# Performance work log

Hardware: AMD Instinct MI355X
Metric: run time of the kernel (lower is better)

## Reference

```python
import jax, jax.numpy as jnp
import numpy as np

STRIDE = 1  # conv stride from __init__


def setup_inputs() -> dict:
    key = jax.random.key(0)
    k1, k2, k3 = jax.random.split(key, 3)
    prot1 = jax.random.normal(k1, (4, 1024, 8, 64), dtype=jnp.float32)
    prot2 = jax.random.normal(k2, (4, 1024, 8, 64), dtype=jnp.float32)
    # W: (no_filters, no_channels, no_dims, window_size)
    W = jax.random.normal(k3, (32, 8, 64, 7), dtype=jnp.float32)
    return {"prot1": prot1, "prot2": prot2, "W": W}


def _project(x, W, stride):
    """Fused equivalent of unfold + broadcast-mul + sum over (C, window).

    x: (N, H, C, D), W: (F, C, D, w) -> (N, F, H', D) with H' = (H - w)//stride + 1.
    This is a grouped 1D conv: D groups, each mixing C input channels into F outputs.
    """
    N, H, C, D = x.shape
    Fn, _, _, w = W.shape
    xg = jnp.transpose(x, (0, 3, 2, 1)).reshape(N, D * C, H)        # (N, D*C, H)
    Wg = jnp.transpose(W, (2, 0, 1, 3)).reshape(D * Fn, C, w)       # (D*F, C, w)
    out = jax.lax.conv_general_dilated(
        xg, Wg, window_strides=(stride,), padding='VALID',
        dimension_numbers=('NCH', 'OIH', 'NCH'), feature_group_count=D)
    Hp = out.shape[-1]
    return jnp.transpose(out.reshape(N, D, Fn, Hp), (0, 2, 3, 1))   # (N, F, H', D)


def reference(prot1, prot2, W):
    q1 = _project(prot1, W, STRIDE)   # (N, F, H1', D)
    q2 = _project(prot2, W, STRIDE)   # (N, F, H2', D)
    H1p, H2p = q1.shape[2], q2.shape[2]
    scale = jnp.sqrt(jnp.asarray(H1p * H2p, dtype=q1.dtype))
    att = jnp.einsum('nfhd,nfgd->nfhg', q1, q2) / scale             # (N, F, H1', H2')
    a = jax.nn.softmax(att, axis=3)
    p1 = jnp.einsum('nfhg,nfgd->nfhd', a, q2)                       # (N, F, H1', D)
    # NB: source does transpose(att, 2, 2) (a no-op) and multiplies the SAME
    # softmax matrix by the UPDATED p1folds; we reproduce that faithfully.
    p2 = jnp.einsum('nfhg,nfgd->nfhd', a, p1)                       # (N, F, H1', D)
    out1 = jnp.tanh(jnp.transpose(p1, (0, 2, 1, 3)))                # (N, H1', F, D)
    out2 = jnp.tanh(jnp.transpose(p2, (0, 2, 1, 3)))
    # Dropout is identity in eval mode (and dropout_p=0.0 here).
    return (out1, out2)
```

## Files before the change

kernel.cpp:

```cpp
#include <hip/hip_runtime.h>
#include <math.h>

typedef __bf16 bf16_t;
typedef bf16_t bf16x4 __attribute__((ext_vector_type(4)));
typedef bf16_t bf16x8 __attribute__((ext_vector_type(8)));
typedef float  f32x16 __attribute__((ext_vector_type(16)));

#define HH 1024
#define CC 8
#define DD 64
#define FF 32
#define WW 7
#define HP 1018
#define HPAD 1024
#define NF 128
#define QOUT (NF*HP*DD)
#define QWS ((size_t)NF*HPAD*DD)

#if __has_builtin(__builtin_amdgcn_exp2f)
#define EXP2(x) __builtin_amdgcn_exp2f(x)
#else
#define EXP2(x) __expf((x) * 0.6931471805599453f)
#endif

#define QSCALE (1.442695040888963f / 1018.f)

__device__ __forceinline__ int vaddr(int row, int col) {
    return row*64 + ((((col>>3) ^ (row&7) ^ ((row>>2)&7)))<<3) + (col&7);
}

__global__ __launch_bounds__(256) void wprep_kernel(
    const float* __restrict__ Wt, float* __restrict__ Wp)
{
    const int idx = blockIdx.x * 256 + threadIdx.x;
    if (idx < FF*CC*DD*WW) {
        const int j = idx % WW;
        int t = idx / WW;
        const int d = t % DD; t /= DD;
        const int c = t % CC;
        const int f = t / CC;
        Wp[((f*CC + c)*WW + j)*DD + d] = Wt[idx];
    }
}

__global__ __launch_bounds__(256, 3) void conv_kernel(
    const float* __restrict__ x1, const float* __restrict__ x2,
    const float* __restrict__ Wp, bf16_t* __restrict__ q1, bf16_t* __restrict__ q2)
{
    __shared__ float xs[22*512];
    const int zin = blockIdx.z & 1;
    const int fh = blockIdx.z >> 1;
    const float* x = zin ? x2 : x1;
    bf16_t* q = zin ? q2 : q1;
    const float qs = zin ? 1.f : QSCALE;
    const int n = blockIdx.y;
    const int hb = blockIdx.x * 16;
    const int tid = threadIdx.x;

    const float4* xg = (const float4*)(x + (size_t)n*HH*512);
    float4* xsv = (float4*)xs;
#pragma unroll
    for (int it = 0; it < 11; ++it) {
        const int i = it*256 + tid;
        const int row = hb + (i >> 7);
        float4 v = {0.f, 0.f, 0.f, 0.f};
        if (row < HH) v = xg[(size_t)row*128 + (i & 127)];
        xsv[i] = v;
    }

    const int d = tid & 63;
    const int fq = tid >> 6;

    float w[2][CC][WW];
#pragma unroll
    for (int fi = 0; fi < 2; ++fi) {
        const int f = fq*8 + fh*2 + fi;
#pragma unroll
        for (int c = 0; c < CC; ++c)
#pragma unroll
            for (int j = 0; j < WW; ++j)
                w[fi][c][j] = Wp[((f*CC + c)*WW + j)*DD + d];
    }

    __syncthreads();

    float acc[2][16];
#pragma unroll
    for (int fi = 0; fi < 2; ++fi)
#pragma unroll
        for (int i = 0; i < 16; ++i) acc[fi][i] = 0.f;

#pragma unroll
    for (int rr = 0; rr < 22; ++rr) {
        float xv[CC];
#pragma unroll
        for (int c = 0; c < CC; ++c)
            xv[c] = xs[rr*512 + c*64 + d];
#pragma unroll
        for (int fi = 0; fi < 2; ++fi)
#pragma unroll
            for (int j = 0; j < WW; ++j) {
                const int i = rr - j;
                if (i >= 0 && i < 16) {
#pragma unroll
                    for (int c = 0; c < CC; ++c)
                        acc[fi][i] = fmaf(xv[c], w[fi][c][j], acc[fi][i]);
                }
            }
    }

#pragma unroll
    for (int fi = 0; fi < 2; ++fi) {
        const int f = fq*8 + fh*2 + fi;
#pragma unroll
        for (int i = 0; i < 16; ++i) {
            const int h = hb + i;
            const float v = (h < HP) ? acc[fi][i]*qs : 0.f;
            q[((size_t)(n*FF + f)*HPAD + h)*DD + d] = (bf16_t)v;
        }
    }
}

__device__ __forceinline__ float fast_tanh(float x) {
    const float t = __expf(2.f * x);
    return (t - 1.f) / (t + 1.f);
}

#define MT_STEP(mtv) {                                                            \
    f32x16 C[2] = {};                                                             \
    __builtin_amdgcn_s_setprio(1);                                                \
    _Pragma("unroll")                                                             \
    for (int kt = 0; kt < 4; ++kt) {                                              \
        C[0] = __builtin_amdgcn_mfma_f32_32x32x16_bf16(aq[mtv][kt], bq1[0][kt], C[0], 0,0,0); \
        C[1] = __builtin_amdgcn_mfma_f32_32x32x16_bf16(aq[mtv][kt], bq1[1][kt], C[1], 0,0,0); \
    }                                                                             \
    __builtin_amdgcn_s_setprio(0);                                                \
    if (g0 + 64 < HPAD) {                                                         \
        _Pragma("unroll")                                                         \
        for (int kt = 0; kt < 4; ++kt)                                            \
            aq[mtv][kt] = *(const bf16x8*)&ap[(size_t)(g0 + 64 + 32*(mtv))*DD + 16*kt]; \
    }                                                                             \
    bf16x8 af[2][2];                                                              \
    _Pragma("unroll")                                                             \
    for (int nt = 0; nt < 2; ++nt) {                                              \
        float ls = 0.f;                                                           \
        _Pragma("unroll")                                                         \
        for (int s = 0; s < 16; ++s) {                                            \
            float e = EXP2(C[nt][s]);                                             \
            if (tail) {                                                           \
                const int gg = g0 + 32*(mtv) + (s&3) + 8*(s>>2) + 4*half;         \
                if (gg >= HP) e = 0.f;                                            \
            }                                                                     \
            ls += e;                                                              \
            af[nt][s>>3][s&7] = (bf16_t)e;                                        \
        }                                                                         \
        lacc[nt] += ls;                                                           \
    }                                                                             \
    __builtin_amdgcn_s_setprio(1);                                                \
    _Pragma("unroll")                                                             \
    for (int u = 0; u < 2; ++u) {                                                 \
        _Pragma("unroll")                                                         \
        for (int dt = 0; dt < 2; ++dt) {                                          \
            const int chunk = (4*(mtv) + 2*u + half) ^ vswz;                      \
            bf16x8 b = *(const bf16x8*)&vtc[(32*dt + lid)*64 + chunk*8];          \
            O[0][dt] = __builtin_amdgcn_mfma_f32_32x32x16_bf16(af[0][u], b, O[0][dt], 0,0,0); \
            O[1][dt] = __builtin_amdgcn_mfma_f32_32x32x16_bf16(af[1][u], b, O[1][dt], 0,0,0); \
        }                                                                         \
    }                                                                             \
    __builtin_amdgcn_s_setprio(0); }

template<int MODE>
__global__ __launch_bounds__(256, 2) void flash(
    const bf16_t* __restrict__ q1, const bf16_t* __restrict__ q2,
    const bf16_t* __restrict__ vsrc, bf16_t* __restrict__ p1out,
    float* __restrict__ out)
{
    __shared__ __align__(16) bf16_t Vt[2][64*64];

    const int head = blockIdx.y;
    const int n = head >> 5, f = head & 31;
    const int tid = threadIdx.x;
    const int w = tid >> 6;
    const int lane = tid & 63;
    const int lid = lane & 31;
    const int half = lane >> 5;
    const int hb = blockIdx.x * 256 + w * 64;
    const bool odd = ((w ^ blockIdx.x ^ blockIdx.y) & 1) != 0;

    const size_t qoff = (size_t)head * HPAD * DD;
    const int vswz = (lid & 7) ^ (lid >> 2);

    const int gq = tid >> 4;
    const int dq = tid & 15;
    const int cgb = 4*((gq>>1)&1) + 8*(gq&1) + 16*(gq>>2);

    const bf16_t* vptr = (MODE == 1) ? vsrc : q2;

    const bf16_t* bp = q1 + qoff + (size_t)(hb + lid)*DD + 8*half;
    const bf16_t* ap = q2 + qoff + (size_t)lid*DD + 8*half;
    const bf16_t* vp = vptr + qoff + (size_t)(4*gq)*DD + 4*dq;

    bf16x8 bq1[2][4];
#pragma unroll
    for (int nt = 0; nt < 2; ++nt)
#pragma unroll
        for (int kt = 0; kt < 4; ++kt)
            bq1[nt][kt] = *(const bf16x8*)&bp[(size_t)(32*nt)*DD + 16*kt];

    bf16x8 aq[2][4];
#pragma unroll
    for (int mt = 0; mt < 2; ++mt)
#pragma unroll
        for (int kt = 0; kt < 4; ++kt)
            aq[mt][kt] = *(const bf16x8*)&ap[(size_t)(32*mt)*DD + 16*kt];

    bf16x4 rV[4];
#pragma unroll
    for (int i = 0; i < 4; ++i)
        rV[i] = *(const bf16x4*)&vp[(size_t)i*DD];
#pragma unroll
    for (int j = 0; j < 4; ++j) {
        bf16x4 c = { rV[0][j], rV[1][j], rV[2][j], rV[3][j] };
        *(bf16x4*)&Vt[0][vaddr(4*dq + j, cgb)] = c;
    }
#pragma unroll
    for (int i = 0; i < 4; ++i)
        rV[i] = *(const bf16x4*)&vp[(size_t)(64 + i)*DD];

    f32x16 O[2][2] = {};
    float lacc[2] = {0.f, 0.f};

    __syncthreads();

    for (int t = 0; t < 16; ++t) {
        const int g0 = t << 6;
        const bf16_t* vtc = Vt[t & 1];

        if (t + 1 < 16) {
            bf16_t* vtn = Vt[(t + 1) & 1];
#pragma unroll
            for (int j = 0; j < 4; ++j) {
                bf16x4 c = { rV[0][j], rV[1][j], rV[2][j], rV[3][j] };
                *(bf16x4*)&vtn[vaddr(4*dq + j, cgb)] = c;
            }
            if (t + 2 < 16) {
#pragma unroll
                for (int i = 0; i < 4; ++i)
                    rV[i] = *(const bf16x4*)&vp[(size_t)((t + 2)*64 + i)*DD];
            }
        }

        const bool tail = (g0 + 64 > HP);

        if (odd) { MT_STEP(1); MT_STEP(0); }
        else     { MT_STEP(0); MT_STEP(1); }

        __syncthreads();
    }

    float linv[2];
#pragma unroll
    for (int nt = 0; nt < 2; ++nt) {
        const float l = lacc[nt] + __shfl_xor(lacc[nt], 32);
        linv[nt] = 1.f / l;
    }
#pragma unroll
    for (int ht = 0; ht < 2; ++ht) {
#pragma unroll
        for (int s = 0; s < 16; ++s) {
            const int R = (s&3) + 8*(s>>2) + 4*half;
            const float li = __shfl(linv[ht], R);
            const int hg = hb + 32*ht + R;
#pragma unroll
            for (int dt = 0; dt < 2; ++dt) {
                const int d = 32*dt + lid;
                const float val = O[ht][dt][s] * li;
                if (hg < HP)
                    out[(((size_t)n*HP + hg)*FF + f)*DD + d] = fast_tanh(val);
                if (MODE == 0)
                    p1out[qoff + (size_t)hg*DD + d] = (bf16_t)(hg < HP ? val : 0.f);
            }
        }
    }
}

extern "C" void kernel_launch(void* const* d_in, const int* in_sizes, int n_in,
                              void* d_out, int out_size, void* d_ws, size_t ws_size,
                              hipStream_t stream)
{
    const float* prot1 = (const float*)d_in[0];
    const float* prot2 = (const float*)d_in[1];
    const float* Wt    = (const float*)d_in[2];
    float* out = (float*)d_out;

    bf16_t* q1b = (bf16_t*)d_ws;
    bf16_t* q2b = q1b + QWS;
    bf16_t* p1b = q2b + QWS;
    float* Wp   = (float*)(p1b + QWS);

    wprep_kernel<<<dim3(448), 256, 0, stream>>>(Wt, Wp);
    conv_kernel<<<dim3(64, 4, 8), 256, 0, stream>>>(prot1, prot2, Wp, q1b, q2b);
    flash<0><<<dim3(4, NF), 256, 0, stream>>>(q1b, q2b, q2b, p1b, out);
    flash<1><<<dim3(4, NF), 256, 0, stream>>>(q1b, q2b, p1b, p1b, out + QOUT);
}
```

Before: 208.6 us.

## Double-buffer Q2 key registers two tiles ahead and swizzle workgroup-to-head mapping

The attention loop is unrolled by two, with separate register sets for alternating key tiles. Each set is prefetched two tiles ahead instead of one, so global load latency gets more time to hide behind MFMA work. The block index is remapped with a swizzle so workgroups sharing a head are spread differently across the grid, which may change L2 and CU locality. The per-wave odd/even ordering of MT_STEP is dropped. Holding extra registers raises register pressure and risks lower occupancy or spills at the 2-blocks-per-CU launch bound.

```diff
diff --git a/kernel.cpp b/kernel.cpp
--- a/kernel.cpp
+++ b/kernel.cpp
@@ -126,19 +126,19 @@
     return (t - 1.f) / (t + 1.f);
 }
 
-#define MT_STEP(mtv) {                                                            \
+#define MT_STEP(AQ, mtv, pft) {                                                   \
     f32x16 C[2] = {};                                                             \
     __builtin_amdgcn_s_setprio(1);                                                \
     _Pragma("unroll")                                                             \
     for (int kt = 0; kt < 4; ++kt) {                                              \
-        C[0] = __builtin_amdgcn_mfma_f32_32x32x16_bf16(aq[mtv][kt], bq1[0][kt], C[0], 0,0,0); \
-        C[1] = __builtin_amdgcn_mfma_f32_32x32x16_bf16(aq[mtv][kt], bq1[1][kt], C[1], 0,0,0); \
+        C[0] = __builtin_amdgcn_mfma_f32_32x32x16_bf16(AQ[mtv][kt], bq1[0][kt], C[0], 0,0,0); \
+        C[1] = __builtin_amdgcn_mfma_f32_32x32x16_bf16(AQ[mtv][kt], bq1[1][kt], C[1], 0,0,0); \
     }                                                                             \
     __builtin_amdgcn_s_setprio(0);                                                \
-    if (g0 + 64 < HPAD) {                                                         \
+    if ((pft) < 16) {          \
         _Pragma("unroll")                                                         \
         for (int kt = 0; kt < 4; ++kt)                                            \
-            aq[mtv][kt] = *(const bf16x8*)&ap[(size_t)(g0 + 64 + 32*(mtv))*DD + 16*kt]; \
+            AQ[mtv][kt] = *(const bf16x8*)&ap[(size_t)((pft)*64 + 32*(mtv))*DD + 16*kt]; \
     }                                                                             \
     bf16x8 af[2][2];                                                              \
     _Pragma("unroll")                                                             \
@@ -169,6 +169,27 @@
     }                                                                             \
     __builtin_amdgcn_s_setprio(0); }
 
+#define TILE_BODY(tt, AQ) {                                                       \
+    const int g0 = (tt) << 6;                                                     \
+    const bf16_t* vtc = Vt[(tt) & 1];                                             \
+    const bool tail = ((tt) == 15);                                               \
+    if ((tt) + 1 < 16) {                                                          \
+        bf16_t* vtn = Vt[((tt) + 1) & 1];                                         \
+        _Pragma("unroll")                                                         \
+        for (int j = 0; j < 4; ++j) {                                             \
+            bf16x4 c = { rV[0][j], rV[1][j], rV[2][j], rV[3][j] };                \
+            *(bf16x4*)&vtn[vaddr(4*dq + j, cgb)] = c;                             \
+        }                                                                         \
+        if ((tt) + 2 < 16) {                                                      \
+            _Pragma("unroll")                                                     \
+            for (int i = 0; i < 4; ++i)                                           \
+                rV[i] = *(const bf16x4*)&vp[(size_t)(((tt) + 2)*64 + i)*DD + 0];  \
+        }                                                                         \
+    }                                                                             \
+    MT_STEP(AQ, 0, (tt) + 2);                                                     \
+    MT_STEP(AQ, 1, (tt) + 2);                                                     \
+    __syncthreads(); }
+
 template<int MODE>
 __global__ __launch_bounds__(256, 2) void flash(
     const bf16_t* __restrict__ q1, const bf16_t* __restrict__ q2,
@@ -177,15 +198,17 @@
 {
     __shared__ __align__(16) bf16_t Vt[2][64*64];
 
-    const int head = blockIdx.y;
+    const int wg = blockIdx.x + 4 * blockIdx.y;
+    const int swz = (wg & 7) * 64 + (wg >> 3);
+    const int head = swz >> 2;
+    const int bx = swz & 3;
     const int n = head >> 5, f = head & 31;
     const int tid = threadIdx.x;
     const int w = tid >> 6;
     const int lane = tid & 63;
     const int lid = lane & 31;
     const int half = lane >> 5;
-    const int hb = blockIdx.x * 256 + w * 64;
-    const bool odd = ((w ^ blockIdx.x ^ blockIdx.y) & 1) != 0;
+    const int hb = bx * 256 + w * 64;
 
     const size_t qoff = (size_t)head * HPAD * DD;
     const int vswz = (lid & 7) ^ (lid >> 2);
@@ -207,12 +230,14 @@
         for (int kt = 0; kt < 4; ++kt)
             bq1[nt][kt] = *(const bf16x8*)&bp[(size_t)(32*nt)*DD + 16*kt];
 
-    bf16x8 aq[2][4];
+    bf16x8 aqA[2][4], aqB[2][4];
 #pragma unroll
     for (int mt = 0; mt < 2; ++mt)
 #pragma unroll
-        for (int kt = 0; kt < 4; ++kt)
-            aq[mt][kt] = *(const bf16x8*)&ap[(size_t)(32*mt)*DD + 16*kt];
+        for (int kt = 0; kt < 4; ++kt) {
+            aqA[mt][kt] = *(const bf16x8*)&ap[(size_t)(32*mt)*DD + 16*kt];
+            aqB[mt][kt] = *(const bf16x8*)&ap[(size_t)(64 + 32*mt)*DD + 16*kt];
+        }
 
     bf16x4 rV[4];
 #pragma unroll
@@ -232,30 +257,9 @@
 
     __syncthreads();
 
-    for (int t = 0; t < 16; ++t) {
-        const int g0 = t << 6;
-        const bf16_t* vtc = Vt[t & 1];
-
-        if (t + 1 < 16) {
-            bf16_t* vtn = Vt[(t + 1) & 1];
-#pragma unroll
-            for (int j = 0; j < 4; ++j) {
-                bf16x4 c = { rV[0][j], rV[1][j], rV[2][j], rV[3][j] };
-                *(bf16x4*)&vtn[vaddr(4*dq + j, cgb)] = c;
-            }
-            if (t + 2 < 16) {
-#pragma unroll
-                for (int i = 0; i < 4; ++i)
-                    rV[i] = *(const bf16x4*)&vp[(size_t)((t + 2)*64 + i)*DD];
-            }
-        }
-
-        const bool tail = (g0 + 64 > HP);
-
-        if (odd) { MT_STEP(1); MT_STEP(0); }
-        else     { MT_STEP(0); MT_STEP(1); }
-
-        __syncthreads();
+    for (int t = 0; t < 16; t += 2) {
+        TILE_BODY(t,     aqA);
+        TILE_BODY(t + 1, aqB);
     }
 
     float linv[2];
```

New measurement: 345.5 us. 65.6% more time.
